# Performance work log

Hardware: AMD Instinct MI355X
Metric: run time of the kernel (lower is better)

The kernel has to match this reference:

```python
import jax, jax.numpy as jnp
import numpy as np

H, W, C, HEADS = 28, 28, 512, 16
N = H * W
FF = 4 * C
DH = C // HEADS
NUM_REL = (2 * H - 1) * W + (2 * W - 1) + 1  # max relative index + 1 (source table is under-sized; see notes)


def _relative_indices():
    ys, xs = np.meshgrid(np.arange(H), np.arange(W), indexing='ij')
    py, px = ys.reshape(-1), xs.reshape(-1)
    # rel[q, k] = (y_k - y_q + H) * W + (x_k - x_q + W), matching the source loop
    rel = (py[None, :] - py[:, None] + H) * W + (px[None, :] - px[:, None] + W)
    return jnp.asarray(rel, dtype=jnp.int32)  # (N, N)


def setup_inputs() -> dict:
    key = jax.random.key(0)
    ks = jax.random.split(key, 9)
    g = lambda k, shape, s: (jax.random.normal(k, shape, jnp.float32) * s)
    return {
        'x': g(ks[0], (16, C, H, W), 1.0),
        'ln_w': jnp.ones((C,), jnp.float32),
        'ln_b': jnp.zeros((C,), jnp.float32),
        'Wq': g(ks[1], (C, C), 0.02), 'bq': jnp.zeros((C,), jnp.float32),
        'Wk': g(ks[2], (C, C), 0.02), 'bk': jnp.zeros((C,), jnp.float32),
        'Wv': g(ks[3], (C, C), 0.02), 'bv': jnp.zeros((C,), jnp.float32),
        'Wo': g(ks[4], (C, C), 0.02), 'bo': jnp.zeros((C,), jnp.float32),
        'rel_bias': g(ks[5], (HEADS, NUM_REL), 0.02),
        'W1': g(ks[6], (C, FF), 0.02), 'b1': jnp.zeros((FF,), jnp.float32),
        'W2': g(ks[7], (FF, C), 0.02), 'b2': jnp.zeros((C,), jnp.float32),
        'rel_idx': _relative_indices(),
    }


def reference(x, ln_w, ln_b, Wq, bq, Wk, bk, Wv, bv, Wo, bo, rel_bias, W1, b1, W2, b2, rel_idx):
    b = x.shape[0]
    xc = jnp.transpose(x, (0, 2, 3, 1)).reshape(b, N, C)  # b n c
    # LayerNorm over channels (per spatial position)
    mu = xc.mean(-1, keepdims=True)
    var = jnp.mean(jnp.square(xc - mu), -1, keepdims=True)
    xn = (xc - mu) * jax.lax.rsqrt(var + 1e-5) * ln_w + ln_b

    split = lambda t: t.reshape(b, N, HEADS, DH).transpose(0, 2, 1, 3)  # b h n d
    q = split(xn @ Wq + bq)
    k = split(xn @ Wk + bk)
    v = split(xn @ Wv + bv)

    bias = rel_bias[:, rel_idx]  # gather -> (heads, n, n)
    scores = jnp.einsum('bhnd,bhmd->bhnm', q, k) + bias[None]  # no 1/sqrt(d), faithful to source
    attn = jax.nn.softmax(scores, axis=-1)
    out = jnp.einsum('bhnm,bhmd->bhnd', attn, v)
    out = out.transpose(0, 2, 1, 3).reshape(b, N, C) @ Wo + bo

    x1 = xc + out  # skip (Identity) + attention branch
    ff = jax.nn.gelu(x1 @ W1 + b1, approximate=False) @ W2 + b2
    x2 = x1 + ff
    return x2.reshape(b, H, W, C).transpose(0, 3, 1, 2)  # back to b c h w
```

## Files before the change

### kernel.cpp

```cpp
#include <hip/hip_runtime.h>
#include <hip/hip_bf16.h>
#include <math.h>
#include <stdint.h>


typedef __bf16 bf16;
typedef __attribute__((ext_vector_type(8))) __bf16 bf16x8;
typedef __attribute__((ext_vector_type(4))) __bf16 bf16x4;
typedef __attribute__((ext_vector_type(4))) float f32x4;

#define NN 784
#define CC 512
#define NHEADS 16
#define DHEAD 32
#define FFD 2048
#define NBATCH 16
#define NREL 1596
#define MFULL (NBATCH * NN)
#define PACKSZ ((size_t)6422528)

__global__ __launch_bounds__(256) void detect_dtype(const unsigned int* xw, int* flag)
{
  __shared__ int cnt[256];
  int plausible = 0;
  for (int i = threadIdx.x; i < 1024; i += 256) {
    unsigned w = xw[i];
    unsigned lo = w & 0xFFFFu;
    unsigned e = (lo >> 7) & 0xFFu;
    if (lo == 0u || (e >= 90u && e <= 140u)) plausible++;
  }
  cnt[threadIdx.x] = plausible;
  __syncthreads();
  if (threadIdx.x == 0) {
    int tot = 0;
    for (int i = 0; i < 256; i++) tot += cnt[i];
    flag[0] = (tot >= 768) ? 1 : 0;
  }
}


__global__ __launch_bounds__(256) void transpose_split_all(
    const float* __restrict__ Wq, const float* __restrict__ Wk,
    const float* __restrict__ Wv, const float* __restrict__ Wo,
    const float* __restrict__ W1, const float* __restrict__ W2,
    bf16* __restrict__ WqkvT_h, bf16* __restrict__ WqkvT_l,
    bf16* __restrict__ WoT_h,   bf16* __restrict__ WoT_l,
    bf16* __restrict__ W1T_h,   bf16* __restrict__ W1T_l,
    bf16* __restrict__ W2T_h,   bf16* __restrict__ W2T_l,
    const int* __restrict__ flag)
{
  if (flag[0] != 0) return;
  int id = blockIdx.x;
  const float* W; bf16 *th, *tl; int K, Nout, roff, nx;
  if (id < 256)       { W = Wq; th = WqkvT_h; tl = WqkvT_l; K = 512;  Nout = 512;  roff = 0;    nx = 16; }
  else if (id < 512)  { W = Wk; th = WqkvT_h; tl = WqkvT_l; K = 512;  Nout = 512;  roff = 512;  nx = 16; id -= 256; }
  else if (id < 768)  { W = Wv; th = WqkvT_h; tl = WqkvT_l; K = 512;  Nout = 512;  roff = 1024; nx = 16; id -= 512; }
  else if (id < 1024) { W = Wo; th = WoT_h;   tl = WoT_l;   K = 512;  Nout = 512;  roff = 0;    nx = 16; id -= 768; }
  else if (id < 2048) { W = W1; th = W1T_h;   tl = W1T_l;   K = 512;  Nout = 2048; roff = 0;    nx = 64; id -= 1024; }
  else                { W = W2; th = W2T_h;   tl = W2T_l;   K = 2048; Nout = 512;  roff = 0;    nx = 16; id -= 2048; }
  const int n0 = (id % nx) * 32, k0 = (id / nx) * 32;

  __shared__ float tile[32][33];
  int tx = threadIdx.x & 31, ty = threadIdx.x >> 5;
  #pragma unroll
  for (int r = 0; r < 32; r += 8)
    tile[ty + r][tx] = W[(size_t)(k0 + ty + r) * Nout + n0 + tx];
  __syncthreads();
  #pragma unroll
  for (int r = 0; r < 32; r += 8) {
    float v = tile[tx][ty + r];
    bf16 h = (bf16)v;
    float lo = v - (float)h;
    size_t idx = (size_t)(roff + n0 + ty + r) * K + k0 + tx;
    th[idx] = h;
    tl[idx] = (bf16)lo;
  }
}

__global__ __launch_bounds__(256) void ln_coal(
    const float* __restrict__ x, const float* __restrict__ lnw,
    const float* __restrict__ lnb, bf16* __restrict__ xh,
    const int* __restrict__ flag)
{
  if (flag[0] != 0) return;
  const int b = blockIdx.y;
  const int n0 = blockIdx.x * 64;
  const int w = threadIdx.x >> 6, l = threadIdx.x & 63;
  const bool act = (n0 + l) < NN;
  int tok = n0 + l; if (tok >= NN) tok = NN - 1;
  const float* xb = x + ((size_t)b * CC + w * 128) * NN + tok;
  float vals[128];
  float s = 0.f, ss = 0.f;
  #pragma unroll
  for (int c = 0; c < 128; c++) {
    float v = xb[(size_t)c * NN];
    vals[c] = v; s += v; ss += v * v;
  }
  __shared__ float S[4][64], SS[4][64];
  S[w][l] = s; SS[w][l] = ss;
  __syncthreads();
  const float St  = S[0][l] + S[1][l] + S[2][l] + S[3][l];
  const float SSt = SS[0][l] + SS[1][l] + SS[2][l] + SS[3][l];
  const float mu  = St * (1.f / 512.f);
  const float var = SSt * (1.f / 512.f) - mu * mu;
  const float rstd = rsqrtf(var + 1e-5f);
  if (act) {
    const size_t row = ((size_t)b * NN + n0 + l) * CC + w * 128;
    #pragma unroll
    for (int cc = 0; cc < 16; cc++) {
      bf16x8 o;
      #pragma unroll
      for (int e = 0; e < 8; e++) {
        const int c = cc * 8 + e;
        o[e] = (bf16)((vals[c] - mu) * rstd * lnw[w * 128 + c] + lnb[w * 128 + c]);
      }
      *(bf16x8*)(xh + row + cc * 8) = o;
    }
  }
}

template <int NOUT, int KD, int ACT, int RESM, int OUTM>
__global__ __launch_bounds__(256) void gemm2(
    const bf16* __restrict__ A,
    const bf16* __restrict__ Bh, const bf16* __restrict__ Bl,
    const float* __restrict__ bias_q, const float* __restrict__ bias_k,
    const float* __restrict__ bias_v,
    float* __restrict__ outf, bf16* __restrict__ out_hi, bf16* __restrict__ out_lo,
    const float* __restrict__ extra_f, const bf16* __restrict__ ex_hi,
    const bf16* __restrict__ ex_lo,
    int M, const int* __restrict__ flag)
{
  if (flag[0] != 0) return;
  __shared__ bf16 sA [2][128 * 32];
  __shared__ bf16 sBh[2][128 * 32];
  __shared__ bf16 sBl[2][128 * 32];
  const int t = threadIdx.x;
  const int lane = t & 63;
  const int w = t >> 6;
  const int wr = w >> 1, wc = w & 1;
  const int lr = lane & 15, kg = lane >> 4;

  const int gx = gridDim.x, gy = gridDim.y;
  const int nwg = gx * gy;
  const int raw = blockIdx.y * gx + blockIdx.x;
  int tile_m, tile_n;
  if ((nwg & 7) == 0 && (gx & 3) == 0 && (gy % 7) == 0) {
    const int q8 = nwg >> 3;
    const int seq = (raw & 7) * q8 + (raw >> 3);
    const int spr = gx >> 2;
    const int s28 = seq / 28, j28 = seq - s28 * 28;
    const int sm = s28 / spr, sn = s28 - sm * spr;
    tile_m = (sm * 7 + (j28 >> 2)) * 128;
    tile_n = (sn * 4 + (j28 & 3)) * 128;
  } else {
    tile_m = blockIdx.y * 128;
    tile_n = blockIdx.x * 128;
  }

  f32x4 acc[4][4];
  #pragma unroll
  for (int m = 0; m < 4; m++)
    #pragma unroll
    for (int n = 0; n < 4; n++) acc[m][n] = (f32x4)0.f;

  const int s0 = t, s1 = t + 256;
  int ar0 = tile_m + (s0 >> 2); if (ar0 >= M) ar0 = M - 1;
  int ar1 = tile_m + (s1 >> 2); if (ar1 >= M) ar1 = M - 1;
  const int br0 = tile_n + (s0 >> 2);
  const int br1 = tile_n + (s1 >> 2);
  const int ac0 = (s0 & 3) * 8, ac1 = (s1 & 3) * 8;
  const size_t a0 = (size_t)ar0 * KD + ac0;
  const size_t a1 = (size_t)ar1 * KD + ac1;
  const size_t b0 = (size_t)br0 * KD + ac0;
  const size_t b1 = (size_t)br1 * KD + ac1;

  #define STAGE(BUF, KO)                                                      \
    do {                                                                      \
      __builtin_amdgcn_global_load_lds(                                       \
          (const __attribute__((address_space(1))) void*)(A + a0 + (KO)),     \
          (__attribute__((address_space(3))) void*)(sA[BUF] + s0 * 8), 16, 0, 0); \
      __builtin_amdgcn_global_load_lds(                                       \
          (const __attribute__((address_space(1))) void*)(A + a1 + (KO)),     \
          (__attribute__((address_space(3))) void*)(sA[BUF] + s1 * 8), 16, 0, 0); \
      __builtin_amdgcn_global_load_lds(                                       \
          (const __attribute__((address_space(1))) void*)(Bh + b0 + (KO)),    \
          (__attribute__((address_space(3))) void*)(sBh[BUF] + s0 * 8), 16, 0, 0); \
      __builtin_amdgcn_global_load_lds(                                       \
          (const __attribute__((address_space(1))) void*)(Bh + b1 + (KO)),    \
          (__attribute__((address_space(3))) void*)(sBh[BUF] + s1 * 8), 16, 0, 0); \
      __builtin_amdgcn_global_load_lds(                                       \
          (const __attribute__((address_space(1))) void*)(Bl + b0 + (KO)),    \
          (__attribute__((address_space(3))) void*)(sBl[BUF] + s0 * 8), 16, 0, 0); \
      __builtin_amdgcn_global_load_lds(                                       \
          (const __attribute__((address_space(1))) void*)(Bl + b1 + (KO)),    \
          (__attribute__((address_space(3))) void*)(sBl[BUF] + s1 * 8), 16, 0, 0); \
    } while (0)

  STAGE(0, 0);
  asm volatile("s_waitcnt vmcnt(0)" ::: "memory");
  __builtin_amdgcn_sched_barrier(0);
  __builtin_amdgcn_s_barrier();
  __builtin_amdgcn_sched_barrier(0);

  int cur = 0;
  for (int k0 = 0; k0 < KD; k0 += 32) {
    if (k0 + 32 < KD) {
      if (cur) STAGE(0, k0 + 32); else STAGE(1, k0 + 32);
    }
    const bf16* pA  = sA [cur];
    const bf16* pBh = sBh[cur];
    const bf16* pBl = sBl[cur];
    bf16x8 af[4], bh[4], bl[4];
    #pragma unroll
    for (int m = 0; m < 4; m++) {
      const int off = (wr * 64 + m * 16 + lr) * 32 + kg * 8;
      af[m] = *(const bf16x8*)(pA + off);
    }
    #pragma unroll
    for (int n = 0; n < 4; n++) {
      const int off = (wc * 64 + n * 16 + lr) * 32 + kg * 8;
      bh[n] = *(const bf16x8*)(pBh + off);
      bl[n] = *(const bf16x8*)(pBl + off);
    }
    #pragma unroll
    for (int m = 0; m < 4; m++)
      #pragma unroll
      for (int n = 0; n < 4; n++) {
        acc[m][n] = __builtin_amdgcn_mfma_f32_16x16x32_bf16(af[m], bh[n], acc[m][n], 0, 0, 0);
        acc[m][n] = __builtin_amdgcn_mfma_f32_16x16x32_bf16(af[m], bl[n], acc[m][n], 0, 0, 0);
      }
    asm volatile("s_waitcnt vmcnt(0)" ::: "memory");
    __builtin_amdgcn_sched_barrier(0);
    __builtin_amdgcn_s_barrier();
    __builtin_amdgcn_sched_barrier(0);
    cur ^= 1;
  }
  #undef STAGE

  #pragma unroll
  for (int m = 0; m < 4; m++) {
    const int r0 = tile_m + wr * 64 + m * 16 + kg * 4;
    #pragma unroll
    for (int n = 0; n < 4; n++) {
      const int cg = tile_n + wc * 64 + n * 16 + lr;
      float bv;
      if (OUTM == 5) {
        const int reg2 = cg >> 9;
        const float* bp = reg2 == 0 ? bias_q : (reg2 == 1 ? bias_k : bias_v);
        bv = bp[cg & 511];
      } else {
        bv = bias_q[cg];
      }
      #pragma unroll
      for (int j = 0; j < 4; j++) {
        const int rg = r0 + j;
        if (rg >= M) continue;
        float vacc = acc[m][n][j] + bv;
        if (ACT == 1) vacc = 0.5f * vacc * (1.f + erff(vacc * 0.70710678118654752f));
        if (RESM == 1) {
          int bl_ = rg / NN, nn = rg - bl_ * NN;
          vacc += extra_f[((size_t)bl_ * CC + cg) * NN + nn];
        }
        if (RESM == 2) {
          size_t ei = (size_t)rg * CC + cg;
          vacc += (float)ex_hi[ei] + (float)ex_lo[ei];
        }
        if (OUTM == 3) {
          size_t oi = (size_t)rg * NOUT + cg;
          bf16 h = (bf16)vacc;
          out_hi[oi] = h;
          out_lo[oi] = (bf16)(vacc - (float)h);
        } else if (OUTM == 4) {
          int bl_ = rg / NN, nn = rg - bl_ * NN;
          outf[((size_t)bl_ * CC + cg) * NN + nn] = vacc;
        } else if (OUTM == 6) {
          out_hi[(size_t)rg * NOUT + cg] = (bf16)vacc;
        } else if (OUTM == 5) {
          const int reg2 = cg >> 9;
          const int c = cg & 511;
          const int hh = c >> 5, dd = c & 31;
          const int bl_ = rg / NN, nn = rg - bl_ * NN;
          const int bh_ = bl_ * NHEADS + hh;
          bf16 h = (bf16)vacc;
          if (reg2 == 0) {
            out_hi[((size_t)bh_ * NN + nn) * 32 + dd] = h;
          } else if (reg2 == 1) {
            out_hi[PACKSZ + ((size_t)bh_ * NN + nn) * 32 + dd] = h;
          } else {
            out_hi[2 * PACKSZ + ((size_t)bh_ * 32 + dd) * NN + nn] = h;
          }
        }
      }
    }
  }
}

__global__ __launch_bounds__(256) void attn_mfma(
    const bf16* __restrict__ pack, const float* __restrict__ relb,
    bf16* __restrict__ o_out, const int* __restrict__ flag)
{
  if (flag[0] != 0) return;
  const int h = blockIdx.y, b = blockIdx.z;
  __shared__ float biasLds[NREL];
  for (int i = threadIdx.x; i < NREL; i += 256) biasLds[i] = relb[(size_t)h * NREL + i];
  __syncthreads();
  const int w = threadIdx.x >> 6, lane = threadIdx.x & 63;
  const int qtile = blockIdx.x * 4 + w;
  if (qtile >= 49) return;
  const int kg = lane >> 4, lq = lane & 15;
  const int qg = qtile * 16 + lq;
  const int bh = b * NHEADS + h;
  const bf16* Q  = pack;
  const bf16* K  = pack + PACKSZ;
  const bf16* Vt = pack + 2 * PACKSZ;
  __shared__ bf16 Plds[4][16][72];

  const bf16x8 qf = *(const bf16x8*)(Q + ((size_t)bh * NN + qg) * 32 + kg * 8);

  float m = -1e30f, l = 0.f;
  f32x4 o0 = (f32x4)0.f, o1 = (f32x4)0.f;
  const float* bb = biasLds + 812 - qg;
  const size_t vrow0 = ((size_t)bh * 32 + lq) * NN;
  const size_t vrow1 = ((size_t)bh * 32 + 16 + lq) * NN;

  for (int c = 0; c < 12; c++) {
    const int c0 = c * 64;
    f32x4 st[4];
    #pragma unroll
    for (int t = 0; t < 4; t++) {
      const int kvr = c0 + t * 16 + lq;
      const bf16x8 kf = *(const bf16x8*)(K + ((size_t)bh * NN + kvr) * 32 + kg * 8);
      st[t] = __builtin_amdgcn_mfma_f32_16x16x32_bf16(kf, qf, (f32x4)0.f, 0, 0, 0);
    }
    float cm = -1e30f;
    #pragma unroll
    for (int t = 0; t < 4; t++)
      #pragma unroll
      for (int r = 0; r < 4; r++) {
        st[t][r] += bb[c0 + t * 16 + 4 * kg + r];
        cm = fmaxf(cm, st[t][r]);
      }
    cm = fmaxf(cm, __shfl_xor(cm, 16));
    cm = fmaxf(cm, __shfl_xor(cm, 32));
    const float mn = fmaxf(m, cm);
    const float al = __expf(m - mn);
    m = mn;
    float cl = 0.f;
    #pragma unroll
    for (int t = 0; t < 4; t++) {
      bf16x4 pk;
      #pragma unroll
      for (int r = 0; r < 4; r++) {
        float p = __expf(st[t][r] - m);
        bf16 pb = (bf16)p;
        pk[r] = pb;
        cl += (float)pb;
      }
      *(bf16x4*)(&Plds[w][lq][t * 16 + 4 * kg]) = pk;
    }
    cl += __shfl_xor(cl, 16);
    cl += __shfl_xor(cl, 32);
    l = l * al + cl;
    #pragma unroll
    for (int r = 0; r < 4; r++) {
      const float ar = __shfl(al, (lane & 48) | (kg * 4 + r));
      o0[r] *= ar; o1[r] *= ar;
    }
    #pragma unroll
    for (int s2 = 0; s2 < 2; s2++) {
      const bf16x8 pa = *(const bf16x8*)(&Plds[w][lq][s2 * 32 + kg * 8]);
      const bf16x8 v0 = *(const bf16x8*)(Vt + vrow0 + c0 + s2 * 32 + kg * 8);
      const bf16x8 v1 = *(const bf16x8*)(Vt + vrow1 + c0 + s2 * 32 + kg * 8);
      o0 = __builtin_amdgcn_mfma_f32_16x16x32_bf16(pa, v0, o0, 0, 0, 0);
      o1 = __builtin_amdgcn_mfma_f32_16x16x32_bf16(pa, v1, o1, 0, 0, 0);
    }
  }

  {
    const int c0 = 768;
    const int kvr = c0 + lq;
    const bf16x8 kf = *(const bf16x8*)(K + ((size_t)bh * NN + kvr) * 32 + kg * 8);
    f32x4 a = __builtin_amdgcn_mfma_f32_16x16x32_bf16(kf, qf, (f32x4)0.f, 0, 0, 0);
    float cm = -1e30f;
    #pragma unroll
    for (int r = 0; r < 4; r++) {
      a[r] += bb[c0 + 4 * kg + r];
      cm = fmaxf(cm, a[r]);
    }
    cm = fmaxf(cm, __shfl_xor(cm, 16));
    cm = fmaxf(cm, __shfl_xor(cm, 32));
    const float mn = fmaxf(m, cm);
    const float al = __expf(m - mn);
    m = mn;
    float cl = 0.f;
    bf16x4 pk, zk;
    #pragma unroll
    for (int r = 0; r < 4; r++) {
      float p = __expf(a[r] - m);
      bf16 pb = (bf16)p;
      pk[r] = pb;
      zk[r] = (bf16)0.f;
      cl += (float)pb;
    }
    *(bf16x4*)(&Plds[w][lq][4 * kg]) = pk;
    *(bf16x4*)(&Plds[w][lq][16 + 4 * kg]) = zk;
    cl += __shfl_xor(cl, 16);
    cl += __shfl_xor(cl, 32);
    l = l * al + cl;
    #pragma unroll
    for (int r = 0; r < 4; r++) {
      const float ar = __shfl(al, (lane & 48) | (kg * 4 + r));
      o0[r] *= ar; o1[r] *= ar;
    }
    bf16x8 vz;
    #pragma unroll
    for (int e = 0; e < 8; e++) vz[e] = (bf16)0.f;
    const int voff = c0 + (kg < 2 ? kg * 8 : 0);
    bf16x8 v0 = *(const bf16x8*)(Vt + vrow0 + voff);
    bf16x8 v1 = *(const bf16x8*)(Vt + vrow1 + voff);
    if (kg >= 2) { v0 = vz; v1 = vz; }
    const bf16x8 pa = *(const bf16x8*)(&Plds[w][lq][kg * 8]);
    o0 = __builtin_amdgcn_mfma_f32_16x16x32_bf16(pa, v0, o0, 0, 0, 0);
    o1 = __builtin_amdgcn_mfma_f32_16x16x32_bf16(pa, v1, o1, 0, 0, 0);
  }

  const float inv = 1.f / l;
  #pragma unroll
  for (int r = 0; r < 4; r++) {
    const float ir = __shfl(inv, (lane & 48) | (kg * 4 + r));
    const int rq = qtile * 16 + kg * 4 + r;
    const size_t oi = ((size_t)b * NN + rq) * CC + h * DHEAD;
    o_out[oi + lq]      = (bf16)(o0[r] * ir);
    o_out[oi + 16 + lq] = (bf16)(o1[r] * ir);
  }
}

static void run_fast_fp32(void* const* d_in, void* d_out, char* base,
                          const int* flag, hipStream_t stream)
{
  const float* x    = (const float*)d_in[0];
  const float* lnw  = (const float*)d_in[1];
  const float* lnb  = (const float*)d_in[2];
  const float* Wq   = (const float*)d_in[3];
  const float* bq   = (const float*)d_in[4];
  const float* Wk   = (const float*)d_in[5];
  const float* bk   = (const float*)d_in[6];
  const float* Wv   = (const float*)d_in[7];
  const float* bv   = (const float*)d_in[8];
  const float* Wo   = (const float*)d_in[9];
  const float* bo   = (const float*)d_in[10];
  const float* relb = (const float*)d_in[11];
  const float* W1   = (const float*)d_in[12];
  const float* b1   = (const float*)d_in[13];
  const float* W2   = (const float*)d_in[14];
  const float* b2   = (const float*)d_in[15];
  float* outp = (float*)d_out;

  bf16* WqkvT_h = (bf16*)(base);
  bf16* WqkvT_l = WqkvT_h + (size_t)1536 * 512;
  bf16* WoT_h   = WqkvT_l + (size_t)1536 * 512;
  bf16* WoT_l   = WoT_h   + (size_t)512 * 512;
  bf16* W1T_h   = WoT_l   + (size_t)512 * 512;
  bf16* W1T_l   = W1T_h   + (size_t)2048 * 512;
  bf16* W2T_h   = W1T_l   + (size_t)2048 * 512;
  bf16* W2T_l   = W2T_h   + (size_t)512 * 2048;
  bf16* xn   = (bf16*)(base + 12582912);
  bf16* qkvp = (bf16*)(base + 25427968);
  bf16* x1_h = (bf16*)(base + 25427968);
  bf16* x1_l = (bf16*)(base + 38273024);
  bf16* ff   = (bf16*)(base + 51118080);
  bf16* at   = xn;

  transpose_split_all<<<dim3(3072), 256, 0, stream>>>(
      Wq, Wk, Wv, Wo, W1, W2,
      WqkvT_h, WqkvT_l, WoT_h, WoT_l, W1T_h, W1T_l, W2T_h, W2T_l, flag);

  const int M = MFULL;
  const int gm = M / 128;

  ln_coal<<<dim3(13, NBATCH), 256, 0, stream>>>(x, lnw, lnb, xn, flag);

  gemm2<1536, 512, 0, 0, 5><<<dim3(12, gm), 256, 0, stream>>>(
      xn, WqkvT_h, WqkvT_l, bq, bk, bv,
      (float*)nullptr, qkvp, (bf16*)nullptr,
      (const float*)nullptr, (const bf16*)nullptr, (const bf16*)nullptr,
      M, flag);

  attn_mfma<<<dim3(13, NHEADS, NBATCH), 256, 0, stream>>>(qkvp, relb, at, flag);

  gemm2<512, 512, 0, 1, 3><<<dim3(4, gm), 256, 0, stream>>>(
      at, WoT_h, WoT_l, bo, (const float*)nullptr, (const float*)nullptr,
      (float*)nullptr, x1_h, x1_l,
      x, (const bf16*)nullptr, (const bf16*)nullptr,
      M, flag);

  gemm2<2048, 512, 1, 0, 6><<<dim3(16, gm), 256, 0, stream>>>(
      x1_h, W1T_h, W1T_l, b1, (const float*)nullptr, (const float*)nullptr,
      (float*)nullptr, ff, (bf16*)nullptr,
      (const float*)nullptr, (const bf16*)nullptr, (const bf16*)nullptr,
      M, flag);

  gemm2<512, 2048, 0, 2, 4><<<dim3(4, gm), 256, 0, stream>>>(
      ff, W2T_h, W2T_l, b2, (const float*)nullptr, (const float*)nullptr,
      outp, (bf16*)nullptr, (bf16*)nullptr,
      (const float*)nullptr, x1_h, x1_l,
      M, flag);
}

template <typename T, int WANT>
__global__ __launch_bounds__(256) void ln_naive(
    const T* __restrict__ x, const T* __restrict__ lnw, const T* __restrict__ lnb,
    T* __restrict__ xn, const int* __restrict__ flag)
{
  if (flag[0] != WANT) return;
  int bn = blockIdx.x;
  int b = bn / NN, n = bn - b * NN;
  const T* xb = x + (size_t)b * CC * NN + n;
  int t = threadIdx.x;
  float v0 = (float)xb[(size_t)t * NN];
  float v1 = (float)xb[(size_t)(t + 256) * NN];
  float s = v0 + v1, ss = v0 * v0 + v1 * v1;
  #pragma unroll
  for (int m = 32; m >= 1; m >>= 1) {
    s  += __shfl_xor(s,  m);
    ss += __shfl_xor(ss, m);
  }
  __shared__ float red[2][4];
  int w = t >> 6, l = t & 63;
  if (l == 0) { red[0][w] = s; red[1][w] = ss; }
  __syncthreads();
  float S  = red[0][0] + red[0][1] + red[0][2] + red[0][3];
  float SS = red[1][0] + red[1][1] + red[1][2] + red[1][3];
  float mu  = S * (1.f / 512.f);
  float var = SS * (1.f / 512.f) - mu * mu;
  float rstd = rsqrtf(var + 1e-5f);
  T* o = xn + (size_t)bn * CC;
  o[t]       = (T)(((v0 - mu) * rstd) * (float)lnw[t]       + (float)lnb[t]);
  o[t + 256] = (T)(((v1 - mu) * rstd) * (float)lnw[t + 256] + (float)lnb[t + 256]);
}

template <typename T, int NOUT, int KD, int ACT, int RESM, int OUTM, int WANT>
__global__ __launch_bounds__(256) void gemm_naive(
    const T* __restrict__ A, const T* __restrict__ W, const T* __restrict__ bias,
    T* __restrict__ out, const T* __restrict__ extra, const int* __restrict__ flag)
{
  if (flag[0] != WANT) return;
  __shared__ float a_t[16][17];
  __shared__ float w_t[16][17];
  int tx = threadIdx.x & 15, ty = threadIdx.x >> 4;
  int m0 = blockIdx.y * 16, bz = blockIdx.z;
  int mg = m0 + ty;
  int jg = blockIdx.x * 16 + tx;
  int ar = mg < NN ? mg : NN - 1;
  const T* Ab = A + (size_t)bz * NN * KD;
  float acc = 0.f;
  for (int k0 = 0; k0 < KD; k0 += 16) {
    a_t[ty][tx] = (float)Ab[(size_t)ar * KD + k0 + tx];
    w_t[ty][tx] = (float)W[(size_t)(k0 + ty) * NOUT + jg];
    __syncthreads();
    #pragma unroll
    for (int kk = 0; kk < 16; kk++)
      acc += a_t[ty][kk] * w_t[kk][tx];
    __syncthreads();
  }
  if (mg >= NN) return;
  acc += (float)bias[jg];
  if (ACT == 1) acc = 0.5f * acc * (1.f + erff(acc * 0.70710678118654752f));
  if (RESM == 1) acc += (float)extra[((size_t)bz * CC + jg) * NN + mg];
  if (RESM == 2) acc += (float)extra[((size_t)bz * NN + mg) * CC + jg];
  if (OUTM == 0) out[((size_t)bz * NN + mg) * NOUT + jg] = (T)acc;
  else           out[((size_t)bz * NOUT + jg) * NN + mg] = (T)acc;
}

template <typename T, int WANT>
__global__ __launch_bounds__(256) void attn_naive(
    const T* __restrict__ q, const T* __restrict__ k, const T* __restrict__ v,
    const T* __restrict__ rel_bias, const int* __restrict__ rel_idx,
    T* __restrict__ attn_out, const int* __restrict__ flag)
{
  if (flag[0] != WANT) return;
  int i = blockIdx.x * 256 + threadIdx.x;
  int h = blockIdx.y, b = blockIdx.z;
  if (i >= NN) return;
  const T* qr = q + ((size_t)b * NN + i) * CC + h * DHEAD;
  float qv[DHEAD];
  #pragma unroll
  for (int d = 0; d < DHEAD; d++) qv[d] = (float)qr[d];
  const int* ridx = rel_idx + (size_t)i * NN;
  const T* rb = rel_bias + (size_t)h * NREL;
  const T* kb = k + (size_t)b * NN * CC + h * DHEAD;
  const T* vb = v + (size_t)b * NN * CC + h * DHEAD;

  float m = -1e30f;
  for (int j = 0; j < NN; j++) {
    const T* kr = kb + (size_t)j * CC;
    float s = 0.f;
    #pragma unroll
    for (int d = 0; d < DHEAD; d++) s += qv[d] * (float)kr[d];
    s += (float)rb[ridx[j]];
    m = fmaxf(m, s);
  }
  float l = 0.f;
  float o[DHEAD];
  #pragma unroll
  for (int d = 0; d < DHEAD; d++) o[d] = 0.f;
  for (int j = 0; j < NN; j++) {
    const T* kr = kb + (size_t)j * CC;
    float s = 0.f;
    #pragma unroll
    for (int d = 0; d < DHEAD; d++) s += qv[d] * (float)kr[d];
    s += (float)rb[ridx[j]];
    float p = __expf(s - m);
    l += p;
    const T* vr = vb + (size_t)j * CC;
    #pragma unroll
    for (int d = 0; d < DHEAD; d++) o[d] += p * (float)vr[d];
  }
  float inv = 1.f / l;
  T* op = attn_out + ((size_t)b * NN + i) * CC + h * DHEAD;
  #pragma unroll
  for (int d = 0; d < DHEAD; d++) op[d] = (T)(o[d] * inv);
}

template <typename T, int WANT>
static void run_pipeline(void* const* d_in, void* d_out, char* buf, int Bc,
                         const int* flag, hipStream_t stream)
{
  const T* x    = (const T*)d_in[0];
  const T* lnw  = (const T*)d_in[1];
  const T* lnb  = (const T*)d_in[2];
  const T* Wq   = (const T*)d_in[3];
  const T* bq   = (const T*)d_in[4];
  const T* Wk   = (const T*)d_in[5];
  const T* bk   = (const T*)d_in[6];
  const T* Wv   = (const T*)d_in[7];
  const T* bv   = (const T*)d_in[8];
  const T* Wo   = (const T*)d_in[9];
  const T* bo   = (const T*)d_in[10];
  const T* relb = (const T*)d_in[11];
  const T* W1   = (const T*)d_in[12];
  const T* b1   = (const T*)d_in[13];
  const T* W2   = (const T*)d_in[14];
  const T* b2   = (const T*)d_in[15];
  const int* reli = (const int*)d_in[16];
  T* outp = (T*)d_out;

  const size_t TOK = (size_t)NN * CC;
  T* xn  = (T*)(buf);
  T* qb  = (T*)(buf + (size_t)Bc * TOK * 4);
  T* kb  = (T*)(buf + 2 * (size_t)Bc * TOK * 4);
  T* vb  = (T*)(buf + 3 * (size_t)Bc * TOK * 4);
  T* ff1 = (T*)(buf + 4 * (size_t)Bc * TOK * 4);
  T* attn_out = xn;
  T* x1 = qb;

  for (int c0 = 0; c0 < NBATCH; c0 += Bc) {
    const T* xc   = x    + (size_t)c0 * CC * NN;
    T*       outc = outp + (size_t)c0 * CC * NN;
    ln_naive<T, WANT><<<dim3(Bc * NN), 256, 0, stream>>>(xc, lnw, lnb, xn, flag);
    gemm_naive<T, CC, CC, 0, 0, 0, WANT><<<dim3(32, 49, Bc), 256, 0, stream>>>(xn, Wq, bq, qb, (const T*)nullptr, flag);
    gemm_naive<T, CC, CC, 0, 0, 0, WANT><<<dim3(32, 49, Bc), 256, 0, stream>>>(xn, Wk, bk, kb, (const T*)nullptr, flag);
    gemm_naive<T, CC, CC, 0, 0, 0, WANT><<<dim3(32, 49, Bc), 256, 0, stream>>>(xn, Wv, bv, vb, (const T*)nullptr, flag);
    attn_naive<T, WANT><<<dim3(4, NHEADS, Bc), 256, 0, stream>>>(qb, kb, vb, relb, reli, attn_out, flag);
    gemm_naive<T, CC, CC, 0, 1, 0, WANT><<<dim3(32, 49, Bc), 256, 0, stream>>>(attn_out, Wo, bo, x1, xc, flag);
    gemm_naive<T, FFD, CC, 1, 0, 0, WANT><<<dim3(128, 49, Bc), 256, 0, stream>>>(x1, W1, b1, ff1, (const T*)nullptr, flag);
    gemm_naive<T, CC, FFD, 0, 2, 1, WANT><<<dim3(32, 49, Bc), 256, 0, stream>>>(ff1, W2, b2, outc, x1, flag);
  }
}

extern "C" void kernel_launch(void* const* d_in, const int* in_sizes, int n_in,
                              void* d_out, int out_size, void* d_ws, size_t ws_size,
                              hipStream_t stream)
{
  int* flag = (int*)d_ws;
  char* base = (char*)d_ws + 256;
  size_t avail = ws_size > 256 ? ws_size - 256 : 0;

  const size_t REQ_FAST = 102498304;
  const size_t PB16 = (size_t)(4 * NN * CC + NN * FFD) * 2;
  const size_t PB32 = (size_t)(4 * NN * CC + NN * FFD) * 4;

  detect_dtype<<<dim3(1), 256, 0, stream>>>((const unsigned int*)d_in[0], flag);

  if (avail >= REQ_FAST) {
    run_fast_fp32(d_in, d_out, base, flag, stream);
  } else {
    int Bc32 = 1;
    for (int c : {16, 8, 4, 2}) {
      if ((size_t)c * PB32 <= avail) { Bc32 = c; break; }
    }
    run_pipeline<float, 0>(d_in, d_out, base, Bc32, flag, stream);
  }

  int Bc16 = 1;
  for (int c : {16, 8, 4, 2}) {
    if ((size_t)c * PB16 <= avail) { Bc16 = c; break; }
  }
  run_pipeline<bf16, 1>(d_in, d_out, base, Bc16, flag, stream);
}
```

Measured before the change: 560.6 us.

## Triple-buffer GEMM LDS staging with prefetch depth two and simplify tile swizzle

Result: slower. 760.6 us (+35.7%).

```diff
diff --git a/kernel.cpp b/kernel.cpp
--- a/kernel.cpp
+++ b/kernel.cpp
@@ -131,31 +131,23 @@
     int M, const int* __restrict__ flag)
 {
   if (flag[0] != 0) return;
-  __shared__ bf16 sA [2][128 * 32];
-  __shared__ bf16 sBh[2][128 * 32];
-  __shared__ bf16 sBl[2][128 * 32];
+  __shared__ bf16 sA [3][128 * 32];
+  __shared__ bf16 sBh[3][128 * 32];
+  __shared__ bf16 sBl[3][128 * 32];
   const int t = threadIdx.x;
   const int lane = t & 63;
   const int w = t >> 6;
   const int wr = w >> 1, wc = w & 1;
   const int lr = lane & 15, kg = lane >> 4;
 
-  const int gx = gridDim.x, gy = gridDim.y;
-  const int nwg = gx * gy;
-  const int raw = blockIdx.y * gx + blockIdx.x;
-  int tile_m, tile_n;
-  if ((nwg & 7) == 0 && (gx & 3) == 0 && (gy % 7) == 0) {
-    const int q8 = nwg >> 3;
-    const int seq = (raw & 7) * q8 + (raw >> 3);
-    const int spr = gx >> 2;
-    const int s28 = seq / 28, j28 = seq - s28 * 28;
-    const int sm = s28 / spr, sn = s28 - sm * spr;
-    tile_m = (sm * 7 + (j28 >> 2)) * 128;
-    tile_n = (sn * 4 + (j28 & 3)) * 128;
-  } else {
-    tile_m = blockIdx.y * 128;
-    tile_n = blockIdx.x * 128;
-  }
+  int wg = blockIdx.y * gridDim.x + blockIdx.x;
+  const int nwg = gridDim.x * gridDim.y;
+  if ((nwg & 7) == 0) {
+    const int cpx = nwg >> 3;
+    wg = (wg & 7) * cpx + (wg >> 3);
+  }
+  const int tile_n = (wg % gridDim.x) * 128;
+  const int tile_m = (wg / gridDim.x) * 128;
 
   f32x4 acc[4][4];
   #pragma unroll
@@ -196,20 +188,27 @@
           (__attribute__((address_space(3))) void*)(sBl[BUF] + s1 * 8), 16, 0, 0); \
     } while (0)
 
+  constexpr int STEPS = KD / 32;
   STAGE(0, 0);
-  asm volatile("s_waitcnt vmcnt(0)" ::: "memory");
-  __builtin_amdgcn_sched_barrier(0);
-  __builtin_amdgcn_s_barrier();
-  __builtin_amdgcn_sched_barrier(0);
-
-  int cur = 0;
-  for (int k0 = 0; k0 < KD; k0 += 32) {
-    if (k0 + 32 < KD) {
-      if (cur) STAGE(0, k0 + 32); else STAGE(1, k0 + 32);
-    }
-    const bf16* pA  = sA [cur];
-    const bf16* pBh = sBh[cur];
-    const bf16* pBl = sBl[cur];
+  STAGE(1, 32);
+
+  for (int s = 0; s < STEPS; s++) {
+    if (s + 1 < STEPS) {
+      asm volatile("s_waitcnt vmcnt(6)" ::: "memory");
+    } else {
+      asm volatile("s_waitcnt vmcnt(0)" ::: "memory");
+    }
+    __builtin_amdgcn_sched_barrier(0);
+    __builtin_amdgcn_s_barrier();
+    __builtin_amdgcn_sched_barrier(0);
+    if (s + 2 < STEPS) {
+      const int nb = (s + 2) % 3;
+      STAGE(nb, (s + 2) * 32);
+    }
+    const int ib = s % 3;
+    const bf16* pA  = sA [ib];
+    const bf16* pBh = sBh[ib];
+    const bf16* pBl = sBl[ib];
     bf16x8 af[4], bh[4], bl[4];
     #pragma unroll
     for (int m = 0; m < 4; m++) {
@@ -229,11 +228,6 @@
         acc[m][n] = __builtin_amdgcn_mfma_f32_16x16x32_bf16(af[m], bh[n], acc[m][n], 0, 0, 0);
         acc[m][n] = __builtin_amdgcn_mfma_f32_16x16x32_bf16(af[m], bl[n], acc[m][n], 0, 0, 0);
       }
-    asm volatile("s_waitcnt vmcnt(0)" ::: "memory");
-    __builtin_amdgcn_sched_barrier(0);
-    __builtin_amdgcn_s_barrier();
-    __builtin_amdgcn_sched_barrier(0);
-    cur ^= 1;
   }
   #undef STAGE
 
```
